# Performance work log

Measured on AMD Instinct MI355X. Metric: run time of the kernel, lower is better.

## Reference

```python
import jax, jax.numpy as jnp
import numpy as np

MAXGRAD = 2.0


def _forward(im, defgrad, affine):
    B, H, W, C = im.shape
    dt = im.dtype
    c = jnp.asarray(MAXGRAD, dt)
    # logistic growth: c / (1 + (c-1) * exp(-x)), maps defgrad into (0, c)
    dg = c / (1.0 + (c - 1.0) * jnp.exp(-defgrad))
    # integral image -> monotone sampling grid
    x_s = jnp.cumsum(dg[..., 0], axis=2)  # cumulate along width
    y_s = jnp.cumsum(dg[..., 1], axis=1)  # cumulate along height
    grid = jnp.stack([x_s, y_s], axis=-1)  # [B,H,W,2]
    # residual affine: affine + identity, applied in homogeneous coords
    ident = jnp.array([1, 0, 0, 0, 1, 0, 0, 0, 1], dtype=dt)
    A = (affine.reshape(-1, 9) + ident).reshape(B, 3, 3)
    grid3 = jnp.concatenate([grid, jnp.ones((B, H, W, 1), dt)], axis=-1)
    grid3 = jnp.einsum('bhwk,bjk->bhwj', grid3, A)  # matmul(grid, A^T)
    x = grid3[..., 0]
    y = grid3[..., 1]
    # bilinear sampling with clamped corner indices
    x0 = jnp.clip(jnp.floor(x).astype(jnp.int32), 0, W - 1)
    x1 = jnp.clip(jnp.floor(x).astype(jnp.int32) + 1, 0, W - 1)
    y0 = jnp.clip(jnp.floor(y).astype(jnp.int32), 0, H - 1)
    y1 = jnp.clip(jnp.floor(y).astype(jnp.int32) + 1, 0, H - 1)
    bidx = jnp.arange(B, dtype=jnp.int32)[:, None, None]  # batch base index
    Ia = im[bidx, y0, x0]  # [B,H,W,C]
    Ib = im[bidx, y1, x0]
    Ic = im[bidx, y0, x1]
    Id = im[bidx, y1, x1]
    x0f = x0.astype(dt); x1f = x1.astype(dt)
    y0f = y0.astype(dt); y1f = y1.astype(dt)
    wa = ((x1f - x) * (y1f - y))[..., None]
    wb = ((x1f - x) * (y - y0f))[..., None]
    wc = ((x - x0f) * (y1f - y))[..., None]
    wd = ((x - x0f) * (y - y0f))[..., None]
    out = wa * Ia + wb * Ib + wc * Ic + wd * Id
    return out, grid3


def setup_inputs() -> dict:
    key = jax.random.key(0)
    k1, k2, k3 = jax.random.split(key, 3)
    B, H, W, C = 16, 512, 512, 4
    im = jax.random.normal(k1, (B, H, W, C), dtype=jnp.float32)
    defgrad = jax.random.normal(k2, (B, H, W, 2), dtype=jnp.float32)
    affine = jax.random.normal(k3, (B, 9), dtype=jnp.float32) * 0.01
    return {"im": im, "defgrad": defgrad, "affine": affine}


def reference(im, defgrad, affine):
    return _forward(im, defgrad, affine)
```

## Files before the change

kernel.cpp:

```cpp
#include <hip/hip_runtime.h>
#include <math.h>

#define BB 16
#define HH 512
#define WW 512
#define CC 4

#define CS_COLS   16
#define CS_CHUNK  128
#define CS_NCHUNK (HH / CS_CHUNK)
#define CS_SEGS   32
#define CS_SEGH   (CS_CHUNK / CS_SEGS)

__global__ __launch_bounds__(512)
void colscan_kernel(const float2* __restrict__ defgrad, float* __restrict__ ys,
                    int ys_stride) {
    const int wt  = blockIdx.x % (WW / CS_COLS);
    const int b   = blockIdx.x / (WW / CS_COLS);
    const int tid = threadIdx.x;

    __shared__ float lds[CS_CHUNK][CS_COLS + 1];
    __shared__ float part[CS_SEGS][CS_COLS];
    __shared__ float carry[2][CS_COLS];

    const int lcol = tid & (CS_COLS - 1);
    const int lrow = tid >> 4;
    const int scol = tid & (CS_COLS - 1);
    const int seg  = tid >> 4;
    const int wcol = wt * CS_COLS + scol;

    if (tid < CS_COLS) carry[0][tid] = 0.f;

    const float2* dg = defgrad + (size_t)b * HH * WW;

    for (int c = 0; c < CS_NCHUNK; ++c) {
#pragma unroll
        for (int k = 0; k < 4; ++k) {
            const int r = lrow + k * 32;
            const int grow = c * CS_CHUNK + r;
            float v = dg[(size_t)grow * WW + wt * CS_COLS + lcol].y;
            lds[r][lcol] = 2.0f / (1.0f + expf(-v));
        }
        __syncthreads();

        float vals[CS_SEGH];
        float s = 0.f;
#pragma unroll
        for (int i = 0; i < CS_SEGH; ++i) {
            vals[i] = lds[seg * CS_SEGH + i][scol];
            s += vals[i];
        }
        part[seg][scol] = s;
        const float cold = carry[c & 1][scol];
        __syncthreads();

        float run = cold, tot = cold;
#pragma unroll
        for (int j = 0; j < CS_SEGS; ++j) {
            float v = part[j][scol];
            tot += v;
            if (j < seg) run += v;
        }
        if (seg == 0) carry[(c + 1) & 1][scol] = tot;

        const size_t gbase =
            ((size_t)(b * HH + c * CS_CHUNK + seg * CS_SEGH) * WW + wcol);
#pragma unroll
        for (int i = 0; i < CS_SEGH; ++i) {
            run += vals[i];
            ys[(gbase + (size_t)i * WW) * (size_t)ys_stride] = run;
        }
        __syncthreads();
    }
}

#define RS_ROWS 4

__global__ __launch_bounds__(512)
void rowscan_sample_kernel(const float4* __restrict__ im4,
                           const float2* __restrict__ defgrad,
                           const float*  __restrict__ affine,
                           const float*  __restrict__ ys, int ys_stride,
                           float4* __restrict__ out4,
                           float*  __restrict__ grid3) {
    const int nwg = BB * (HH / RS_ROWS);
    const int cpx = nwg / 8;
    const int l   = (blockIdx.x & 7) * cpx + (blockIdx.x >> 3);
    const int hb  = l % (HH / RS_ROWS);
    const int b   = l / (HH / RS_ROWS);
    const int h0  = hb * RS_ROWS;

    const int w    = threadIdx.x;
    const int lane = w & 63;
    const int wv   = w >> 6;

    const size_t imgbase  = (size_t)b * HH * WW;
    const size_t rowbase0 = imgbase + (size_t)h0 * WW + w;

    float dgx[RS_ROWS], ysv[RS_ROWS];
#pragma unroll
    for (int r = 0; r < RS_ROWS; ++r) {
        const size_t pix = rowbase0 + (size_t)r * WW;
        dgx[r] = defgrad[pix].x;
        ysv[r] = ys[pix * (size_t)ys_stride];
    }
#pragma unroll
    for (int r = 0; r < RS_ROWS; ++r)
        dgx[r] = 2.0f / (1.0f + expf(-dgx[r]));

    float x0 = dgx[0], x1 = dgx[1], x2 = dgx[2], x3 = dgx[3];
#pragma unroll
    for (int off = 1; off < 64; off <<= 1) {
        float n0 = __shfl_up(x0, off, 64);
        float n1 = __shfl_up(x1, off, 64);
        float n2 = __shfl_up(x2, off, 64);
        float n3 = __shfl_up(x3, off, 64);
        if (lane >= off) { x0 += n0; x1 += n1; x2 += n2; x3 += n3; }
    }
    __shared__ float wsum[8][RS_ROWS];
    if (lane == 63) {
        wsum[wv][0] = x0; wsum[wv][1] = x1; wsum[wv][2] = x2; wsum[wv][3] = x3;
    }
    __syncthreads();
    float p0 = 0.f, p1 = 0.f, p2 = 0.f, p3 = 0.f;
    for (int j = 0; j < wv; ++j) {
        p0 += wsum[j][0]; p1 += wsum[j][1]; p2 += wsum[j][2]; p3 += wsum[j][3];
    }
    float xs[RS_ROWS] = { x0 + p0, x1 + p1, x2 + p2, x3 + p3 };

    const float* Ab = affine + b * 9;
    const float a00 = Ab[0] + 1.f, a01 = Ab[1], a02 = Ab[2];
    const float a10 = Ab[3], a11 = Ab[4] + 1.f, a12 = Ab[5];
    const float a20 = Ab[6], a21 = Ab[7], a22 = Ab[8] + 1.f;

#pragma unroll
    for (int r = 0; r < RS_ROWS; ++r) {
        const size_t pix = rowbase0 + (size_t)r * WW;
        const float xg = a00 * xs[r] + a01 * ysv[r] + a02;
        const float yg = a10 * xs[r] + a11 * ysv[r] + a12;
        const float wg = a20 * xs[r] + a21 * ysv[r] + a22;

        const int ix = (int)floorf(xg);
        const int iy = (int)floorf(yg);
        const int cx0 = min(max(ix,     0), WW - 1);
        const int cx1 = min(max(ix + 1, 0), WW - 1);
        const int cy0 = min(max(iy,     0), HH - 1);
        const int cy1 = min(max(iy + 1, 0), HH - 1);
        const float x0f = (float)cx0, x1f = (float)cx1;
        const float y0f = (float)cy0, y1f = (float)cy1;
        const float wa = (x1f - xg) * (y1f - yg);
        const float wb = (x1f - xg) * (yg - y0f);
        const float wc = (xg - x0f) * (y1f - yg);
        const float wd = (xg - x0f) * (yg - y0f);

        const float4 Ia = im4[imgbase + (size_t)cy0 * WW + cx0];
        const float4 Ib = im4[imgbase + (size_t)cy1 * WW + cx0];
        const float4 Ic = im4[imgbase + (size_t)cy0 * WW + cx1];
        const float4 Id = im4[imgbase + (size_t)cy1 * WW + cx1];

        float4 o;
        o.x = wa * Ia.x + wb * Ib.x + wc * Ic.x + wd * Id.x;
        o.y = wa * Ia.y + wb * Ib.y + wc * Ic.y + wd * Id.y;
        o.z = wa * Ia.z + wb * Ib.z + wc * Ic.z + wd * Id.z;
        o.w = wa * Ia.w + wb * Ib.w + wc * Ic.w + wd * Id.w;
        out4[pix] = o;

        grid3[pix * 3 + 0] = xg;
        grid3[pix * 3 + 1] = yg;
        grid3[pix * 3 + 2] = wg;
    }
}

extern "C" void kernel_launch(void* const* d_in, const int* in_sizes, int n_in,
                              void* d_out, int out_size, void* d_ws, size_t ws_size,
                              hipStream_t stream) {
    const float* im      = (const float*)d_in[0];
    const float* defgrad = (const float*)d_in[1];
    const float* affine  = (const float*)d_in[2];

    float* out   = (float*)d_out;
    float* grid3 = out + (size_t)BB * HH * WW * CC;

    const size_t ys_bytes = (size_t)BB * HH * WW * sizeof(float);
    float* ys;
    int ys_stride;
    if (ws_size >= ys_bytes) {
        ys = (float*)d_ws;
        ys_stride = 1;
    } else {
        ys = grid3 + 1;
        ys_stride = 3;
    }

    colscan_kernel<<<BB * (WW / CS_COLS), 512, 0, stream>>>(
        (const float2*)defgrad, ys, ys_stride);

    rowscan_sample_kernel<<<BB * (HH / RS_ROWS), 512, 0, stream>>>(
        (const float4*)im, (const float2*)defgrad, affine,
        ys, ys_stride, (float4*)out, grid3);
}
```

Baseline: 250.2 us.

## Precompute x logistic in column scan and batch gather loads in sampler

The column-scan kernel now reads the full float2 defgrad and writes the transformed x component into a second workspace plane when the workspace is large enough. The sampler then reads that plane instead of the strided defgrad x component and skips the exp. The column scan widens to 32 columns with 1024 threads, and the sampler issues all sixteen gathers before doing the blends, with a launch-bounds occupancy hint. This trades an extra full-plane write and read for coalesced reads and more gathers in flight, and it only takes effect if the workspace holds two planes.

```diff
diff --git a/kernel.cpp b/kernel.cpp
--- a/kernel.cpp
+++ b/kernel.cpp
@@ -6,40 +6,42 @@
 #define WW 512
 #define CC 4
 
-#define CS_COLS   16
-#define CS_CHUNK  128
-#define CS_NCHUNK (HH / CS_CHUNK)
-#define CS_SEGS   32
-#define CS_SEGH   (CS_CHUNK / CS_SEGS)
-
-__global__ __launch_bounds__(512)
-void colscan_kernel(const float2* __restrict__ defgrad, float* __restrict__ ys,
-                    int ys_stride) {
+#define CS_COLS    32
+#define CS_THREADS 1024
+#define CS_SEGS    (CS_THREADS / CS_COLS)
+#define CS_CHUNK   128
+#define CS_SEGH    (CS_CHUNK / CS_SEGS)
+#define CS_NCHUNK  (HH / CS_CHUNK)
+
+__global__ __launch_bounds__(CS_THREADS)
+void colscan_kernel(const float2* __restrict__ defgrad,
+                    float* __restrict__ ys, int ys_stride,
+                    float* __restrict__ dgx) {
     const int wt  = blockIdx.x % (WW / CS_COLS);
     const int b   = blockIdx.x / (WW / CS_COLS);
     const int tid = threadIdx.x;
+    const int col = tid & (CS_COLS - 1);
+    const int seg = tid >> 5;
 
     __shared__ float lds[CS_CHUNK][CS_COLS + 1];
     __shared__ float part[CS_SEGS][CS_COLS];
     __shared__ float carry[2][CS_COLS];
 
-    const int lcol = tid & (CS_COLS - 1);
-    const int lrow = tid >> 4;
-    const int scol = tid & (CS_COLS - 1);
-    const int seg  = tid >> 4;
-    const int wcol = wt * CS_COLS + scol;
-
     if (tid < CS_COLS) carry[0][tid] = 0.f;
 
-    const float2* dg = defgrad + (size_t)b * HH * WW;
+    const size_t ibase = (size_t)b * HH * WW + wt * CS_COLS;
 
     for (int c = 0; c < CS_NCHUNK; ++c) {
 #pragma unroll
         for (int k = 0; k < 4; ++k) {
-            const int r = lrow + k * 32;
+            const int r    = seg + k * 32;
             const int grow = c * CS_CHUNK + r;
-            float v = dg[(size_t)grow * WW + wt * CS_COLS + lcol].y;
-            lds[r][lcol] = 2.0f / (1.0f + expf(-v));
+            const size_t gi = ibase + (size_t)grow * WW + col;
+            float2 v = defgrad[gi];
+            float lx = 2.0f / (1.0f + expf(-v.x));
+            float ly = 2.0f / (1.0f + expf(-v.y));
+            if (dgx) dgx[gi] = lx;
+            lds[r][col] = ly;
         }
         __syncthreads();
 
@@ -47,28 +49,28 @@
         float s = 0.f;
 #pragma unroll
         for (int i = 0; i < CS_SEGH; ++i) {
-            vals[i] = lds[seg * CS_SEGH + i][scol];
+            vals[i] = lds[seg * CS_SEGH + i][col];
             s += vals[i];
         }
-        part[seg][scol] = s;
-        const float cold = carry[c & 1][scol];
+        part[seg][col] = s;
+        const float cold = carry[c & 1][col];
         __syncthreads();
 
         float run = cold, tot = cold;
 #pragma unroll
         for (int j = 0; j < CS_SEGS; ++j) {
-            float v = part[j][scol];
+            float v = part[j][col];
             tot += v;
             if (j < seg) run += v;
         }
-        if (seg == 0) carry[(c + 1) & 1][scol] = tot;
-
-        const size_t gbase =
-            ((size_t)(b * HH + c * CS_CHUNK + seg * CS_SEGH) * WW + wcol);
+        if (seg == 0) carry[(c + 1) & 1][col] = tot;
+
+        const size_t gidx0 =
+            (size_t)(b * HH + c * CS_CHUNK + seg * CS_SEGH) * WW + wt * CS_COLS + col;
 #pragma unroll
         for (int i = 0; i < CS_SEGH; ++i) {
             run += vals[i];
-            ys[(gbase + (size_t)i * WW) * (size_t)ys_stride] = run;
+            ys[(gidx0 + (size_t)i * WW) * (size_t)ys_stride] = run;
         }
         __syncthreads();
     }
@@ -76,11 +78,12 @@
 
 #define RS_ROWS 4
 
-__global__ __launch_bounds__(512)
+__global__ __launch_bounds__(512, 4)
 void rowscan_sample_kernel(const float4* __restrict__ im4,
                            const float2* __restrict__ defgrad,
                            const float*  __restrict__ affine,
                            const float*  __restrict__ ys, int ys_stride,
+                           const float*  __restrict__ dgxp,
                            float4* __restrict__ out4,
                            float*  __restrict__ grid3) {
     const int nwg = BB * (HH / RS_ROWS);
@@ -97,18 +100,27 @@
     const size_t imgbase  = (size_t)b * HH * WW;
     const size_t rowbase0 = imgbase + (size_t)h0 * WW + w;
 
-    float dgx[RS_ROWS], ysv[RS_ROWS];
-#pragma unroll
-    for (int r = 0; r < RS_ROWS; ++r) {
-        const size_t pix = rowbase0 + (size_t)r * WW;
-        dgx[r] = defgrad[pix].x;
-        ysv[r] = ys[pix * (size_t)ys_stride];
-    }
-#pragma unroll
-    for (int r = 0; r < RS_ROWS; ++r)
-        dgx[r] = 2.0f / (1.0f + expf(-dgx[r]));
-
-    float x0 = dgx[0], x1 = dgx[1], x2 = dgx[2], x3 = dgx[3];
+    float dgxv[RS_ROWS], ysv[RS_ROWS];
+    if (dgxp) {
+#pragma unroll
+        for (int r = 0; r < RS_ROWS; ++r) {
+            const size_t pix = rowbase0 + (size_t)r * WW;
+            dgxv[r] = dgxp[pix];
+            ysv[r]  = ys[pix];
+        }
+    } else {
+#pragma unroll
+        for (int r = 0; r < RS_ROWS; ++r) {
+            const size_t pix = rowbase0 + (size_t)r * WW;
+            dgxv[r] = defgrad[pix].x;
+            ysv[r]  = ys[pix * (size_t)ys_stride];
+        }
+#pragma unroll
+        for (int r = 0; r < RS_ROWS; ++r)
+            dgxv[r] = 2.0f / (1.0f + expf(-dgxv[r]));
+    }
+
+    float x0 = dgxv[0], x1 = dgxv[1], x2 = dgxv[2], x3 = dgxv[3];
 #pragma unroll
     for (int off = 1; off < 64; off <<= 1) {
         float n0 = __shfl_up(x0, off, 64);
@@ -133,41 +145,55 @@
     const float a10 = Ab[3], a11 = Ab[4] + 1.f, a12 = Ab[5];
     const float a20 = Ab[6], a21 = Ab[7], a22 = Ab[8] + 1.f;
 
+    float xg[RS_ROWS], yg[RS_ROWS], wgv[RS_ROWS];
+    int   offA[RS_ROWS], offB[RS_ROWS], offC[RS_ROWS], offD[RS_ROWS];
+    float wa[RS_ROWS], wb[RS_ROWS], wc[RS_ROWS], wd[RS_ROWS];
 #pragma unroll
     for (int r = 0; r < RS_ROWS; ++r) {
-        const size_t pix = rowbase0 + (size_t)r * WW;
-        const float xg = a00 * xs[r] + a01 * ysv[r] + a02;
-        const float yg = a10 * xs[r] + a11 * ysv[r] + a12;
-        const float wg = a20 * xs[r] + a21 * ysv[r] + a22;
-
-        const int ix = (int)floorf(xg);
-        const int iy = (int)floorf(yg);
+        xg[r]  = a00 * xs[r] + a01 * ysv[r] + a02;
+        yg[r]  = a10 * xs[r] + a11 * ysv[r] + a12;
+        wgv[r] = a20 * xs[r] + a21 * ysv[r] + a22;
+
+        const int ix = (int)floorf(xg[r]);
+        const int iy = (int)floorf(yg[r]);
         const int cx0 = min(max(ix,     0), WW - 1);
         const int cx1 = min(max(ix + 1, 0), WW - 1);
         const int cy0 = min(max(iy,     0), HH - 1);
         const int cy1 = min(max(iy + 1, 0), HH - 1);
         const float x0f = (float)cx0, x1f = (float)cx1;
         const float y0f = (float)cy0, y1f = (float)cy1;
-        const float wa = (x1f - xg) * (y1f - yg);
-        const float wb = (x1f - xg) * (yg - y0f);
-        const float wc = (xg - x0f) * (y1f - yg);
-        const float wd = (xg - x0f) * (yg - y0f);
-
-        const float4 Ia = im4[imgbase + (size_t)cy0 * WW + cx0];
-        const float4 Ib = im4[imgbase + (size_t)cy1 * WW + cx0];
-        const float4 Ic = im4[imgbase + (size_t)cy0 * WW + cx1];
-        const float4 Id = im4[imgbase + (size_t)cy1 * WW + cx1];
-
+        wa[r] = (x1f - xg[r]) * (y1f - yg[r]);
+        wb[r] = (x1f - xg[r]) * (yg[r] - y0f);
+        wc[r] = (xg[r] - x0f) * (y1f - yg[r]);
+        wd[r] = (xg[r] - x0f) * (yg[r] - y0f);
+        offA[r] = cy0 * WW + cx0;
+        offB[r] = cy1 * WW + cx0;
+        offC[r] = cy0 * WW + cx1;
+        offD[r] = cy1 * WW + cx1;
+    }
+
+    float4 Ia[RS_ROWS], Ib[RS_ROWS], Ic[RS_ROWS], Id[RS_ROWS];
+#pragma unroll
+    for (int r = 0; r < RS_ROWS; ++r) {
+        Ia[r] = im4[imgbase + (size_t)offA[r]];
+        Ib[r] = im4[imgbase + (size_t)offB[r]];
+        Ic[r] = im4[imgbase + (size_t)offC[r]];
+        Id[r] = im4[imgbase + (size_t)offD[r]];
+    }
+
+#pragma unroll
+    for (int r = 0; r < RS_ROWS; ++r) {
+        const size_t pix = rowbase0 + (size_t)r * WW;
         float4 o;
-        o.x = wa * Ia.x + wb * Ib.x + wc * Ic.x + wd * Id.x;
-        o.y = wa * Ia.y + wb * Ib.y + wc * Ic.y + wd * Id.y;
-        o.z = wa * Ia.z + wb * Ib.z + wc * Ic.z + wd * Id.z;
-        o.w = wa * Ia.w + wb * Ib.w + wc * Ic.w + wd * Id.w;
+        o.x = wa[r] * Ia[r].x + wb[r] * Ib[r].x + wc[r] * Ic[r].x + wd[r] * Id[r].x;
+        o.y = wa[r] * Ia[r].y + wb[r] * Ib[r].y + wc[r] * Ic[r].y + wd[r] * Id[r].y;
+        o.z = wa[r] * Ia[r].z + wb[r] * Ib[r].z + wc[r] * Ic[r].z + wd[r] * Id[r].z;
+        o.w = wa[r] * Ia[r].w + wb[r] * Ib[r].w + wc[r] * Ic[r].w + wd[r] * Id[r].w;
         out4[pix] = o;
 
-        grid3[pix * 3 + 0] = xg;
-        grid3[pix * 3 + 1] = yg;
-        grid3[pix * 3 + 2] = wg;
+        grid3[pix * 3 + 0] = xg[r];
+        grid3[pix * 3 + 1] = yg[r];
+        grid3[pix * 3 + 2] = wgv[r];
     }
 }
 
@@ -181,21 +207,28 @@
     float* out   = (float*)d_out;
     float* grid3 = out + (size_t)BB * HH * WW * CC;
 
-    const size_t ys_bytes = (size_t)BB * HH * WW * sizeof(float);
-    float* ys;
-    int ys_stride;
-    if (ws_size >= ys_bytes) {
-        ys = (float*)d_ws;
+    const size_t plane_elems = (size_t)BB * HH * WW;
+    const size_t plane_bytes = plane_elems * sizeof(float);
+
+    float* ysp;
+    int    ys_stride;
+    float* dgxp = nullptr;
+    if (ws_size >= 2 * plane_bytes) {
+        ysp = (float*)d_ws;
+        ys_stride = 1;
+        dgxp = (float*)d_ws + plane_elems;
+    } else if (ws_size >= plane_bytes) {
+        ysp = (float*)d_ws;
         ys_stride = 1;
     } else {
-        ys = grid3 + 1;
+        ysp = grid3 + 1;
         ys_stride = 3;
     }
 
-    colscan_kernel<<<BB * (WW / CS_COLS), 512, 0, stream>>>(
-        (const float2*)defgrad, ys, ys_stride);
+    colscan_kernel<<<BB * (WW / CS_COLS), CS_THREADS, 0, stream>>>(
+        (const float2*)defgrad, ysp, ys_stride, dgxp);
 
     rowscan_sample_kernel<<<BB * (HH / RS_ROWS), 512, 0, stream>>>(
         (const float4*)im, (const float2*)defgrad, affine,
-        ys, ys_stride, (float4*)out, grid3);
+        ysp, ys_stride, dgxp, (float4*)out, grid3);
 }
```

After: 259.2 us. +3.6%, slower.
